# Performance work log

Hardware: AMD Instinct MI355X
Metric: run time of the kernel (lower is better)

The kernel has to match this reference:

```python
import jax, jax.numpy as jnp
import numpy as np
from jax import lax

# dims
B, S, NF, E = 128, 256, 32, 4
D, H = 256, 4
DI = 2 * D            # mLSTM inner (up-projection) dim
DHM, DHS = DI // H, D // H
K = 4                 # causal conv kernel size
FF = 352              # gated FFN dim (~4/3 * D, sLSTM block post-FFN)
NE, NP = 100, 6


def _ln(x, g, b, eps=1e-5):
    mu = x.mean(-1, keepdims=True)
    v = x.var(-1, keepdims=True)
    return (x - mu) / jnp.sqrt(v + eps) * g + b


def _cconv(x, w, b):
    # depthwise causal conv1d: x [B,S,C], w [K,C], b [C]
    k = w.shape[0]
    xp = jnp.pad(x, ((0, 0), (k - 1, 0), (0, 0)))
    y = lax.conv_general_dilated(xp, w[:, None, :], (1,), 'VALID',
                                 dimension_numbers=('NWC', 'WIO', 'NWC'),
                                 feature_group_count=x.shape[-1])
    return y + b


def _headnorm(x, g, b, eps=1e-6):
    # per-head group norm: normalize over last (head-dim) axis
    mu = x.mean(-1, keepdims=True)
    v = x.var(-1, keepdims=True)
    return (x - mu) / jnp.sqrt(v + eps) * g + b


def _forward(emb_esn, emb_prof, W_in, b_in,
             m_ln_g, m_ln_b, m_Wup, m_bup, m_convW, m_convb,
             m_Wq, m_bq, m_Wk, m_bk, m_Wv, m_bv,
             m_Wi, m_bi, m_Wf, m_bf, m_skip, m_ng, m_nb, m_Wdown, m_bdown,
             s_ln_g, s_ln_b, s_convW, s_convb,
             s_Wi, s_bi, s_Wf, s_bf, s_Wz, s_bz, s_Wo, s_bo,
             s_Ri, s_Rf, s_Rz, s_Ro, s_ng, s_nb,
             f_ln_g, f_ln_b, f_Wup, f_bup, f_Wdown, f_bdown,
             h_W1, h_b1, h_W2, h_b2,
             x_sens, x_esn, x_prof):
    Bx, Sx = x_sens.shape[0], x_sens.shape[1]
    ve = jnp.broadcast_to(emb_esn[x_esn][:, None, :], (Bx, Sx, E))
    vp = jnp.broadcast_to(emb_prof[x_prof][:, None, :], (Bx, Sx, E))
    x = jnp.concatenate([x_sens, ve, vp], -1) @ W_in + b_in  # [B,S,D]

    # ---------------- block 0: mLSTM (parallel stabilized matrix memory) ----
    xn = _ln(x, m_ln_g, m_ln_b)
    up = xn @ m_Wup + m_bup
    xm, zg = jnp.split(up, 2, axis=-1)              # [B,S,DI] each
    a = jax.nn.silu(_cconv(xm, m_convW, m_convb))   # causal conv + SiLU
    q = a @ m_Wq + m_bq
    k = a @ m_Wk + m_bk
    v = xm @ m_Wv + m_bv
    gin = jnp.concatenate([q, k, v], -1)            # [B,S,3*DI]
    ipre = (gin @ m_Wi + m_bi).transpose(0, 2, 1)   # [B,H,S]
    fpre = (gin @ m_Wf + m_bf).transpose(0, 2, 1)

    def heads(t, dh):
        return t.reshape(Bx, Sx, H, dh).transpose(0, 2, 1, 3)
    qh, kh, vh = heads(q, DHM), heads(k, DHM), heads(v, DHM)  # [B,H,S,dh]

    lfg = jax.nn.log_sigmoid(fpre)
    F = jnp.cumsum(lfg, -1)                         # [B,H,S]
    logD = F[:, :, :, None] - F[:, :, None, :] + ipre[:, :, None, :]
    mask = jnp.tril(jnp.ones((Sx, Sx), bool))
    logD = jnp.where(mask, logD, -jnp.inf)
    mstab = logD.max(-1, keepdims=True)             # [B,H,S,1]
    Dm = jnp.exp(logD - mstab)
    scores = jnp.einsum('bhtd,bhsd->bhts', qh, kh) / np.sqrt(DHM).astype(np.float32)
    C = scores * Dm
    nrm = jnp.maximum(jnp.abs(C.sum(-1, keepdims=True)), jnp.exp(-mstab))
    hh = jnp.einsum('bhts,bhsd->bhtd', C, vh) / nrm
    hn = _headnorm(hh, m_ng.reshape(1, H, 1, DHM), m_nb.reshape(1, H, 1, DHM))
    hn = hn.transpose(0, 2, 1, 3).reshape(Bx, Sx, DI)
    hn = hn + m_skip * a                            # learnable skip from conv branch
    x = x + (hn * jax.nn.silu(zg)) @ m_Wdown + m_bdown

    # ---------------- block 1: sLSTM (stabilized scalar recurrent scan) -----
    xn = _ln(x, s_ln_g, s_ln_b)
    ac = jax.nn.silu(_cconv(xn, s_convW, s_convb))
    to_t = lambda t: t.reshape(Bx, Sx, H, DHS).transpose(1, 0, 2, 3)  # [S,B,H,dh]
    it = to_t(ac @ s_Wi + s_bi)
    ft = to_t(ac @ s_Wf + s_bf)
    zt = to_t(xn @ s_Wz + s_bz)
    ot = to_t(xn @ s_Wo + s_bo)

    def step(carry, xs):
        h, c, n, m = carry
        i0, f0, z0, o0 = xs
        ip = i0 + jnp.einsum('bhd,hde->bhe', h, s_Ri)
        fp = f0 + jnp.einsum('bhd,hde->bhe', h, s_Rf)
        zp = jnp.tanh(z0 + jnp.einsum('bhd,hde->bhe', h, s_Rz))
        op = jax.nn.sigmoid(o0 + jnp.einsum('bhd,hde->bhe', h, s_Ro))
        mn = jnp.maximum(fp + m, ip)
        ig = jnp.exp(ip - mn)
        fg = jnp.exp(fp + m - mn)
        c = fg * c + ig * zp
        n = fg * n + ig
        h = op * c / n
        return (h, c, n, mn), h

    init = tuple(jnp.zeros((Bx, H, DHS), x.dtype) for _ in range(4))
    _, hs = lax.scan(step, init, (it, ft, zt, ot))  # hs [S,B,H,dh]
    hs = _headnorm(hs, s_ng.reshape(1, 1, H, DHS), s_nb.reshape(1, 1, H, DHS))
    x = x + hs.transpose(1, 0, 2, 3).reshape(Bx, Sx, D)

    # gated FFN (sLSTM block post-feedforward)
    xn = _ln(x, f_ln_g, f_ln_b)
    g_, u_ = jnp.split(xn @ f_Wup + f_bup, 2, axis=-1)
    x = x + (jax.nn.gelu(g_) * u_) @ f_Wdown + f_bdown

    last = x[:, -1, :]
    return jax.nn.relu(last @ h_W1 + h_b1) @ h_W2 + h_b2


def setup_inputs() -> dict:
    key = jax.random.key(0)
    ks = iter(jax.random.split(key, 64))
    nrm = lambda sh, s=0.02: jax.random.normal(next(ks), sh, jnp.float32) * s
    z = lambda sh: jnp.zeros(sh, jnp.float32)
    o = lambda sh: jnp.ones(sh, jnp.float32)
    return dict(
        x_sens=jax.random.normal(next(ks), (B, S, NF), jnp.float32),
        x_esn=jax.random.randint(next(ks), (B,), 0, NE, jnp.int32),
        x_prof=jax.random.randint(next(ks), (B,), 0, NP, jnp.int32),
        emb_esn=nrm((NE + 1, E)), emb_prof=nrm((NP + 1, E)),
        W_in=nrm((NF + 2 * E, D)), b_in=z((D,)),
        m_ln_g=o((D,)), m_ln_b=z((D,)),
        m_Wup=nrm((D, 2 * DI)), m_bup=z((2 * DI,)),
        m_convW=nrm((K, DI)), m_convb=z((DI,)),
        m_Wq=nrm((DI, DI)), m_bq=z((DI,)),
        m_Wk=nrm((DI, DI)), m_bk=z((DI,)),
        m_Wv=nrm((DI, DI)), m_bv=z((DI,)),
        m_Wi=nrm((3 * DI, H)), m_bi=z((H,)),
        m_Wf=nrm((3 * DI, H)), m_bf=o((H,)),
        m_skip=o((DI,)), m_ng=o((DI,)), m_nb=z((DI,)),
        m_Wdown=nrm((DI, D)), m_bdown=z((D,)),
        s_ln_g=o((D,)), s_ln_b=z((D,)),
        s_convW=nrm((K, D)), s_convb=z((D,)),
        s_Wi=nrm((D, D)), s_bi=z((D,)),
        s_Wf=nrm((D, D)), s_bf=o((D,)),
        s_Wz=nrm((D, D)), s_bz=z((D,)),
        s_Wo=nrm((D, D)), s_bo=z((D,)),
        s_Ri=nrm((H, DHS, DHS)), s_Rf=nrm((H, DHS, DHS)),
        s_Rz=nrm((H, DHS, DHS)), s_Ro=nrm((H, DHS, DHS)),
        s_ng=o((D,)), s_nb=z((D,)),
        f_ln_g=o((D,)), f_ln_b=z((D,)),
        f_Wup=nrm((D, 2 * FF)), f_bup=z((2 * FF,)),
        f_Wdown=nrm((FF, D)), f_bdown=z((D,)),
        h_W1=nrm((D, 64), 0.05), h_b1=z((64,)),
        h_W2=nrm((64, 3), 0.05), h_b2=z((3,)),
    )


def reference(emb_esn, emb_prof, W_in, b_in,
              m_ln_g, m_ln_b, m_Wup, m_bup, m_convW, m_convb,
              m_Wq, m_bq, m_Wk, m_bk, m_Wv, m_bv,
              m_Wi, m_bi, m_Wf, m_bf, m_skip, m_ng, m_nb, m_Wdown, m_bdown,
              s_ln_g, s_ln_b, s_convW, s_convb,
              s_Wi, s_bi, s_Wf, s_bf, s_Wz, s_bz, s_Wo, s_bo,
              s_Ri, s_Rf, s_Rz, s_Ro, s_ng, s_nb,
              f_ln_g, f_ln_b, f_Wup, f_bup, f_Wdown, f_bdown,
              h_W1, h_b1, h_W2, h_b2,
              x_sens, x_esn, x_prof):
    return _forward(emb_esn, emb_prof, W_in, b_in,
                    m_ln_g, m_ln_b, m_Wup, m_bup, m_convW, m_convb,
                    m_Wq, m_bq, m_Wk, m_bk, m_Wv, m_bv,
                    m_Wi, m_bi, m_Wf, m_bf, m_skip, m_ng, m_nb, m_Wdown, m_bdown,
                    s_ln_g, s_ln_b, s_convW, s_convb,
                    s_Wi, s_bi, s_Wf, s_bf, s_Wz, s_bz, s_Wo, s_bo,
                    s_Ri, s_Rf, s_Rz, s_Ro, s_ng, s_nb,
                    f_ln_g, f_ln_b, f_Wup, f_bup, f_Wdown, f_bdown,
                    h_W1, h_b1, h_W2, h_b2,
                    x_sens, x_esn, x_prof)
```

## Files before the change

kernel.cpp:

```cpp
#include <hip/hip_runtime.h>
#include <cstdint>
#include <cstddef>


using u16 = unsigned short;
using u32 = unsigned int;

typedef __attribute__((ext_vector_type(8))) short short8;
typedef __attribute__((ext_vector_type(8))) unsigned short ushort8v;
typedef __attribute__((ext_vector_type(4))) float float4v;

#define DEVINL __device__ __forceinline__

DEVINL float b2f(u16 u){ u32 x = ((u32)u) << 16; return __builtin_bit_cast(float, x); }
DEVINL u16 f2b(float f){
  u32 x = __builtin_bit_cast(u32, f);
  u32 r = x + 0x7FFFu + ((x >> 16) & 1u);
  return (u16)(r >> 16);
}
DEVINL float ldval(float x){ return x; }
DEVINL float ldval(u16 x){ return b2f(x); }
DEVINL void stval(float* p, float v){ *p = v; }
DEVINL void stval(u16* p, float v){ *p = f2b(v); }

constexpr int IN_N = 56;
constexpr long long IN_SIZES[IN_N] = {
  1048576, 128, 128, 404, 28, 10240, 256, 256, 256,
  262144, 1024, 2048, 512,
  262144, 512, 262144, 512, 262144, 512,
  6144, 4, 6144, 4,
  512, 512, 512, 131072, 256,
  256, 256, 1024, 256,
  65536, 256, 65536, 256, 65536, 256, 65536, 256,
  16384, 16384, 16384, 16384,
  256, 256,
  256, 256, 180224, 704, 90112, 256,
  16384, 64, 192, 3 };

constexpr bool is_wt_input(int i){
  return i==9 || i==13 || i==15 || i==17 || i==26 || i==32 || i==34 || i==36
      || i==38 || i==48 || i==50;
}

struct CvOff { long long off[IN_N+1]; };
constexpr CvOff make_off(){
  CvOff o{};
  long long a = 0;
  for (int i = 0; i < IN_N; i++){
    o.off[i] = a;
    long long s = IN_SIZES[i];
    if (i == 1 || i == 2 || is_wt_input(i)) s = 0;
    a += s;
  }
  o.off[IN_N] = a;
  return o;
}
constexpr CvOff CVOFF = make_off();
constexpr long long CV_TOTAL = CVOFF.off[IN_N];

constexpr int WT_NW = 11;
constexpr int WTB_IN[WT_NW] = {9, 13, 15, 17, 26, 32, 34, 36, 38, 48, 50};
constexpr int WTB_K[WT_NW]  = {256,512,512,512,512,256,256,256,256,256,352};
constexpr int WTB_N[WT_NW]  = {1024,512,512,512,256,256,256,256,256,704,256};
constexpr long long WTO[WT_NW+1] = {0, 262144, 524288, 786432, 1048576, 1179648,
  1245184, 1310720, 1376256, 1441792, 1622016, 1712128};
constexpr long long WT_ELEMS = WTO[WT_NW];

constexpr long long alignup(long long x){ return ((x + 255) / 256) * 256; }
constexpr long long TOK = 32768;
constexpr long long OFF_FLAG = alignup(CV_TOTAL);
constexpr long long OFF_IP  = OFF_FLAG + 64;
constexpr long long OFF_FP  = OFF_IP  + 131072;
constexpr long long OFF_F   = OFF_FP  + 131072;
constexpr long long OFF_G   = OFF_F   + 131072;
constexpr long long OFF_M   = OFF_G   + 131072;
constexpr long long OFF_X   = OFF_M   + 131072;
constexpr long long OFF_XN  = OFF_X   + TOK*256;
constexpr long long OFF_UP  = OFF_XN  + TOK*128;
constexpr long long OFF_A   = OFF_UP  + TOK*512;
constexpr long long OFF_Q   = OFF_A   + TOK*256;
constexpr long long OFF_K   = OFF_Q   + TOK*256;
constexpr long long OFF_V   = OFF_K   + TOK*256;
constexpr long long OFF_WT  = OFF_V   + TOK*256;
constexpr long long WS_END  = OFF_WT  + WT_ELEMS/2 + 256;


__global__ void detect_kernel(const void* mlng, int* flag){
  if (threadIdx.x == 0){
    u32 u = *(const u32*)mlng;
    *flag = (u == 0x3F803F80u) ? 1 : 0;
  }
}

struct InPtrs { const void* p[IN_N]; };

__global__ __launch_bounds__(256) void convert_kernel(InPtrs ptrs, float* __restrict__ cv,
                                                      const int* __restrict__ flag){
  long long gid = (long long)blockIdx.x * 256 + threadIdx.x;
  if (gid >= CV_TOTAL) return;
  int seg = 0;
#pragma unroll
  for (int i = 1; i < IN_N; i++) seg += (gid >= CVOFF.off[i]) ? 1 : 0;
  long long local = gid - CVOFF.off[seg];
  float v;
  if (*flag) v = b2f(((const u16*)ptrs.p[seg])[local]);
  else       v = ((const float*)ptrs.p[seg])[local];
  cv[gid] = v;
}

__global__ __launch_bounds__(256) void wtrans_kernel(InPtrs ptrs, u16* __restrict__ WTb,
                                                     const int* __restrict__ flag){
  int wz = blockIdx.z;
  int K = WTB_K[wz], N = WTB_N[wz];
  int n0 = blockIdx.x * 32, k0 = blockIdx.y * 32;
  if (n0 >= N || k0 >= K) return;
  const void* W = ptrs.p[WTB_IN[wz]];
  u16* WT = WTb + WTO[wz];
  __shared__ u16 tile[32][34];
  int tx = threadIdx.x & 31, ty = threadIdx.x >> 5;
  bool bf = (*flag != 0);
#pragma unroll
  for (int i = 0; i < 4; i++){
    size_t src = (size_t)(k0 + ty + i*8)*N + n0 + tx;
    tile[ty + i*8][tx] = bf ? ((const u16*)W)[src] : f2b(((const float*)W)[src]);
  }
  __syncthreads();
#pragma unroll
  for (int i = 0; i < 4; i++)
    WT[(size_t)(n0 + ty + i*8)*K + k0 + tx] = tile[tx][ty + i*8];
}

__global__ __launch_bounds__(256) void cat_kernel(const float* __restrict__ xs,
    const int* __restrict__ xe, const int* __restrict__ xp,
    const float* __restrict__ ee, const float* __restrict__ ep,
    float* __restrict__ CAT){
  int gid = blockIdx.x * 256 + threadIdx.x;
  int c = gid % 40; int t = gid / 40; int b = t >> 8;
  float v;
  if (c < 32)      v = xs[(size_t)t*32 + c];
  else if (c < 36) v = ee[xe[b]*4 + (c - 32)];
  else             v = ep[xp[b]*4 + (c - 36)];
  CAT[(size_t)t*40 + c] = v;
}

template<typename TA, typename TC>
__global__ __launch_bounds__(256) void gemm_kernel(
    const TA* __restrict__ A, int lda,
    const float* __restrict__ Wm, const float* __restrict__ bias,
    TC* __restrict__ Cc, int ldc, const float* __restrict__ resid,
    int M, int N, int K)
{
  __shared__ float As[16][68];
  __shared__ float Bs[16][68];
  const int bm = blockIdx.y * 64, bn = blockIdx.x * 64;
  const int tid = threadIdx.x, tx = tid & 15, ty = tid >> 4;
  float acc[4][4] = {};
  for (int k0 = 0; k0 < K; k0 += 16){
#pragma unroll
    for (int i = 0; i < 4; i++){
      int idx = tid + i*256;
      int m = idx >> 4, kq = idx & 15;
      As[kq][m] = (k0 + kq < K) ? ldval(A[(size_t)(bm + m)*lda + k0 + kq]) : 0.f;
      int kk = idx >> 6, n = idx & 63;
      Bs[kk][n] = (k0 + kk < K) ? Wm[(size_t)(k0 + kk)*N + bn + n] : 0.f;
    }
    __syncthreads();
#pragma unroll
    for (int kq = 0; kq < 16; kq++){
      float av[4], bv[4];
#pragma unroll
      for (int i = 0; i < 4; i++) av[i] = As[kq][ty*4 + i];
#pragma unroll
      for (int j = 0; j < 4; j++) bv[j] = Bs[kq][tx*4 + j];
#pragma unroll
      for (int i = 0; i < 4; i++)
#pragma unroll
        for (int j = 0; j < 4; j++) acc[i][j] += av[i]*bv[j];
    }
    __syncthreads();
  }
#pragma unroll
  for (int i = 0; i < 4; i++){
    int m = bm + ty*4 + i;
#pragma unroll
    for (int j = 0; j < 4; j++){
      int n = bn + tx*4 + j;
      float v = acc[i][j] + bias[n];
      if (resid) v += resid[(size_t)m*ldc + n];
      stval(&Cc[(size_t)m*ldc + n], v);
    }
  }
}

template<typename TC>
__global__ __launch_bounds__(256) void gemm_mfma(
    const u16* __restrict__ A, int lda,
    const u16* __restrict__ WT,
    const float* __restrict__ bias,
    TC* __restrict__ Cc, int ldc, const float* __restrict__ resid,
    int N, int K)
{
  __shared__ alignas(16) u16 As[128*40];
  __shared__ alignas(16) u16 Bs[128*40];
  const int bm = blockIdx.y * 128, bn = blockIdx.x * 128;
  const int tid = threadIdx.x;
  const int w = tid >> 6, lane = tid & 63, lm = lane & 15, q = lane >> 4;
  const int wm = w >> 1, wn = w & 1;
  float4v acc[4][4] = {};
  for (int k0 = 0; k0 < K; k0 += 32){
    __syncthreads();
#pragma unroll
    for (int c = tid; c < 512; c += 256){
      int r = c >> 2, ch = c & 3;
      *(uint4*)&As[r*40 + ch*8] = *(const uint4*)&A[(size_t)(bm + r)*lda + k0 + ch*8];
      int n = bn + r;
      uint4 bv = {0u,0u,0u,0u};
      if (n < N) bv = *(const uint4*)&WT[(size_t)n*K + k0 + ch*8];
      *(uint4*)&Bs[r*40 + ch*8] = bv;
    }
    __syncthreads();
    short8 a[4], b[4];
#pragma unroll
    for (int i = 0; i < 4; i++)
      a[i] = *(const short8*)&As[(wm*64 + i*16 + lm)*40 + q*8];
#pragma unroll
    for (int j = 0; j < 4; j++)
      b[j] = *(const short8*)&Bs[(wn*64 + j*16 + lm)*40 + q*8];
#pragma unroll
    for (int i = 0; i < 4; i++)
#pragma unroll
      for (int j = 0; j < 4; j++)
        acc[i][j] = __builtin_amdgcn_mfma_f32_16x16x32_bf16(a[i], b[j], acc[i][j], 0, 0, 0);
  }
#pragma unroll
  for (int i = 0; i < 4; i++){
#pragma unroll
    for (int j = 0; j < 4; j++){
      int col = bn + wn*64 + j*16 + lm;
      if (col < N){
#pragma unroll
        for (int r = 0; r < 4; r++){
          int row = bm + wm*64 + i*16 + q*4 + r;
          float v = acc[i][j][r] + bias[col];
          if (resid) v += resid[(size_t)row*ldc + col];
          stval(&Cc[(size_t)row*ldc + col], v);
        }
      }
    }
  }
}

__global__ __launch_bounds__(256) void ln_kernel(const float* __restrict__ Xin,
    const float* __restrict__ g, const float* __restrict__ b,
    u16* __restrict__ out, float eps){
  int t = blockIdx.x*4 + (threadIdx.x >> 6);
  int e = threadIdx.x & 63;
  float4 v = *(const float4*)&Xin[(size_t)t*256 + e*4];
  float su = v.x + v.y + v.z + v.w;
#pragma unroll
  for (int o = 32; o > 0; o >>= 1) su += __shfl_xor(su, o, 64);
  float mu = su * (1.f/256.f);
  float d0 = v.x - mu, d1 = v.y - mu, d2 = v.z - mu, d3 = v.w - mu;
  float sq = d0*d0 + d1*d1 + d2*d2 + d3*d3;
#pragma unroll
  for (int o = 32; o > 0; o >>= 1) sq += __shfl_xor(sq, o, 64);
  float rstd = rsqrtf(sq * (1.f/256.f) + eps);
  float4 gv = *(const float4*)&g[e*4];
  float4 bv = *(const float4*)&b[e*4];
  ushort4 o4;
  o4.x = f2b(d0*rstd*gv.x + bv.x);
  o4.y = f2b(d1*rstd*gv.y + bv.y);
  o4.z = f2b(d2*rstd*gv.z + bv.z);
  o4.w = f2b(d3*rstd*gv.w + bv.w);
  *(ushort4*)&out[(size_t)t*256 + e*4] = o4;
}

__global__ __launch_bounds__(256) void conv_silu_kernel(const u16* __restrict__ Xc, int ldx, int C,
    const float* __restrict__ w, const float* __restrict__ bias, u16* __restrict__ Y){
  int nc = C >> 3;
  long long gid = (long long)blockIdx.x * 256 + threadIdx.x;
  int c8 = (int)(gid % nc) * 8; long long t = gid / nc;
  int s = (int)(t & 255);
  float acc[8];
#pragma unroll
  for (int i = 0; i < 8; i++) acc[i] = bias[c8 + i];
#pragma unroll
  for (int j = 0; j < 4; j++){
    int so = s - 3 + j;
    if (so >= 0){
      ushort8v xv = *(const ushort8v*)&Xc[(size_t)(t - 3 + j)*ldx + c8];
#pragma unroll
      for (int i = 0; i < 8; i++) acc[i] += b2f(xv[i]) * w[j*C + c8 + i];
    }
  }
  ushort8v o8;
#pragma unroll
  for (int i = 0; i < 8; i++) o8[i] = f2b(acc[i] / (1.f + __expf(-acc[i])));
  *(ushort8v*)&Y[(size_t)t*C + c8] = o8;
}

__global__ __launch_bounds__(256) void gates_kernel(
    const u16* __restrict__ Q, const u16* __restrict__ Kb, const u16* __restrict__ V,
    const float* __restrict__ Wi, const float* __restrict__ bi,
    const float* __restrict__ Wf, const float* __restrict__ bf,
    float* __restrict__ IP, float* __restrict__ FP){
  int t = blockIdx.x; int tid = threadIdx.x;
  int o = tid & 7, seg = tid >> 3;
  int b = t >> 8, s = t & 255;
  int g = o & 3;
  const float* Wg = (o >= 4) ? Wf : Wi;
  float part = 0.f;
#pragma unroll
  for (int i = 0; i < 6; i++){
    int k8 = seg*48 + i*8;
    const u16* src; int off;
    if (k8 < 512){ src = Q; off = k8; }
    else if (k8 < 1024){ src = Kb; off = k8 - 512; }
    else { src = V; off = k8 - 1024; }
    ushort8v gv = *(const ushort8v*)&src[(size_t)t*512 + off];
#pragma unroll
    for (int j = 0; j < 8; j++) part += b2f(gv[j]) * Wg[(k8 + j)*4 + g];
  }
  __shared__ float red[256];
  red[tid] = part; __syncthreads();
  if (tid < 8){
    float tot = 0.f;
    for (int ss = 0; ss < 32; ss++) tot += red[ss*8 + tid];
    int gg = tid & 3;
    if (tid < 4) IP[(b*4 + gg)*256 + s] = tot + bi[gg];
    else         FP[(b*4 + gg)*256 + s] = tot + bf[gg];
  }
}

__global__ __launch_bounds__(256) void fscan_kernel(const float* __restrict__ IP,
    const float* __restrict__ FP, float* __restrict__ Fo, float* __restrict__ Go,
    float* __restrict__ Mo){
  int bh = blockIdx.x; int s = threadIdx.x;
  int idx = bh*256 + s;
  __shared__ float buf[256];
  float fp = FP[idx];
  float lfg = fminf(fp, 0.f) - log1pf(expf(-fabsf(fp)));
  float v = lfg;
  buf[s] = v; __syncthreads();
  for (int off = 1; off < 256; off <<= 1){
    float tv = (s >= off) ? buf[s - off] : 0.f;
    __syncthreads();
    v += tv; buf[s] = v;
    __syncthreads();
  }
  float Fv = v;
  float g = IP[idx] - Fv;
  float mv = g;
  buf[s] = mv; __syncthreads();
  for (int off = 1; off < 256; off <<= 1){
    float tv = (s >= off) ? buf[s - off] : -3.0e38f;
    __syncthreads();
    mv = fmaxf(mv, tv); buf[s] = mv;
    __syncthreads();
  }
  Fo[idx] = Fv; Go[idx] = g; Mo[idx] = mv;
}

__global__ __launch_bounds__(256) void attn_kernel(
    const u16* __restrict__ Q, const u16* __restrict__ Kb, const u16* __restrict__ V,
    const float* __restrict__ G, const float* __restrict__ Mx, const float* __restrict__ F,
    const u16* __restrict__ Ab, const u16* __restrict__ UPb,
    const float* __restrict__ ng, const float* __restrict__ nb,
    const float* __restrict__ skip, u16* __restrict__ Yb)
{
  int bh = blockIdx.y, b = bh >> 2, h = bh & 3;
  int tt = blockIdx.x, t0 = tt * 64;
  int tid = threadIdx.x;
  int w = tid >> 6, lane = tid & 63, lm = lane & 15, q = lane >> 4;
  int gbase = bh * 256;

  __shared__ alignas(16) u16 Qs[64*136];
  __shared__ alignas(16) u16 Ks[64*136];
  __shared__ alignas(16) u16 Vt[128*72];
  __shared__ alignas(16) u16 Ps[64*72];
  __shared__ float rs[64];

#pragma unroll
  for (int c = tid; c < 1024; c += 256){
    int r = c >> 4, ch = c & 15;
    *(uint4*)&Qs[r*136 + ch*8] =
      *(const uint4*)&Q[((size_t)(b*256 + t0 + r))*512 + h*128 + ch*8];
  }
  if (tid < 64) rs[tid] = 0.f;

  float mrow[4];
#pragma unroll
  for (int r = 0; r < 4; r++) mrow[r] = Mx[gbase + t0 + w*16 + q*4 + r];

  float4v acc2[8] = {};
  const float scale = 0.08838834764831845f;

  for (int ss = 0; ss <= tt; ss++){
    int s0 = ss * 64;
    __syncthreads();
#pragma unroll
    for (int c = tid; c < 1024; c += 256){
      int r = c >> 4, ch = c & 15;
      *(uint4*)&Ks[r*136 + ch*8] =
        *(const uint4*)&Kb[((size_t)(b*256 + s0 + r))*512 + h*128 + ch*8];
    }
#pragma unroll
    for (int c = tid; c < 1024; c += 256){
      int sl = c & 63, db = c >> 6;
      ushort8v v = *(const ushort8v*)&V[((size_t)(b*256 + s0 + sl))*512 + h*128 + db*8];
#pragma unroll
      for (int j = 0; j < 8; j++) Vt[(db*8 + j)*72 + sl] = v[j];
    }
    __syncthreads();
    float4v sacc[4] = {};
#pragma unroll
    for (int k0 = 0; k0 < 128; k0 += 32){
      short8 a = *(const short8*)&Qs[(w*16 + lm)*136 + k0 + q*8];
#pragma unroll
      for (int j = 0; j < 4; j++){
        short8 bb = *(const short8*)&Ks[(j*16 + lm)*136 + k0 + q*8];
        sacc[j] = __builtin_amdgcn_mfma_f32_16x16x32_bf16(a, bb, sacc[j], 0, 0, 0);
      }
    }
    float rp[4] = {0.f, 0.f, 0.f, 0.f};
#pragma unroll
    for (int j = 0; j < 4; j++){
      int scol = s0 + j*16 + lm;
      float gq = G[gbase + scol];
#pragma unroll
      for (int r = 0; r < 4; r++){
        int trow = t0 + w*16 + q*4 + r;
        float cval = (scol <= trow) ? sacc[j][r]*scale*__expf(gq - mrow[r]) : 0.f;
        Ps[(w*16 + q*4 + r)*72 + j*16 + lm] = f2b(cval);
        rp[r] += cval;
      }
    }
#pragma unroll
    for (int r = 0; r < 4; r++){
#pragma unroll
      for (int m = 1; m < 16; m <<= 1) rp[r] += __shfl_xor(rp[r], m, 16);
      if (lm == 0) rs[w*16 + q*4 + r] += rp[r];
    }
#pragma unroll
    for (int k0 = 0; k0 < 64; k0 += 32){
      short8 a = *(const short8*)&Ps[(w*16 + lm)*72 + k0 + q*8];
#pragma unroll
      for (int jd = 0; jd < 8; jd++){
        short8 bb = *(const short8*)&Vt[(jd*16 + lm)*72 + k0 + q*8];
        acc2[jd] = __builtin_amdgcn_mfma_f32_16x16x32_bf16(a, bb, acc2[jd], 0, 0, 0);
      }
    }
  }
  __syncthreads();
#pragma unroll
  for (int r = 0; r < 4; r++){
    int rl = w*16 + q*4 + r;
    int t = t0 + rl;
    float Fv = F[gbase + t];
    float nrm = fmaxf(fabsf(rs[rl]), __expf(-(Fv + mrow[r])));
    float inv = 1.f / nrm;
    float vv[8];
    float su = 0.f;
#pragma unroll
    for (int jd = 0; jd < 8; jd++){ vv[jd] = acc2[jd][r]*inv; su += vv[jd]; }
#pragma unroll
    for (int m = 1; m < 16; m <<= 1) su += __shfl_xor(su, m, 16);
    float mu = su * (1.f/128.f);
    float sq = 0.f;
#pragma unroll
    for (int jd = 0; jd < 8; jd++){ vv[jd] -= mu; sq += vv[jd]*vv[jd]; }
#pragma unroll
    for (int m = 1; m < 16; m <<= 1) sq += __shfl_xor(sq, m, 16);
    float rstd = rsqrtf(sq * (1.f/128.f) + 1e-6f);
#pragma unroll
    for (int jd = 0; jd < 8; jd++){
      int c = h*128 + jd*16 + lm;
      float hv = vv[jd]*rstd*ng[c] + nb[c];
      float av = b2f(Ab[(size_t)t*512 + c]);
      float zg = b2f(UPb[(size_t)t*1024 + 512 + c]);
      float sz = zg / (1.f + __expf(-zg));
      Yb[(size_t)t*512 + c] = f2b((hv + skip[c]*av)*sz);
    }
  }
}

__global__ __launch_bounds__(320) void scan_kernel(
    const float* __restrict__ IT, const float* __restrict__ FT,
    const float* __restrict__ ZT, const float* __restrict__ OT,
    const float* __restrict__ Ri, const float* __restrict__ Rf,
    const float* __restrict__ Rz, const float* __restrict__ Ro,
    const float* __restrict__ sng, const float* __restrict__ snb,
    float* __restrict__ Xr){
  int bh = blockIdx.x; int b = bh >> 2, h = bh & 3;
  int e = threadIdx.x & 63;
  int w = threadIdx.x >> 6;
  __shared__ float4 part[2][4][64];
  __shared__ float hbuf[2][64];
  size_t rowbase = ((size_t)b*256)*256 + h*64 + e;

  if (w < 4){
    float r0[16], r1[16], r2[16], r3[16];
    const float* Rp0 = Ri + h*4096 + w*1024;
    const float* Rp1 = Rf + h*4096 + w*1024;
    const float* Rp2 = Rz + h*4096 + w*1024;
    const float* Rp3 = Ro + h*4096 + w*1024;
#pragma unroll
    for (int d = 0; d < 16; d++){
      r0[d] = Rp0[d*64 + e];
      r1[d] = Rp1[d*64 + e];
      r2[d] = Rp2[d*64 + e];
      r3[d] = Rp3[d*64 + e];
    }
    float hS = 0.f, cS = 0.f, nS = 0.f, mS = 0.f;
    float i0 = 0.f, f0 = 0.f, z0 = 0.f, o0 = 0.f;
    if (w == 0){ i0 = IT[rowbase]; f0 = FT[rowbase]; z0 = ZT[rowbase]; o0 = OT[rowbase]; }
    for (int s = 0; s < 256; s++){
      float iN = 0.f, fN = 0.f, zN = 0.f, oN = 0.f;
      if (w == 0 && s < 255){
        size_t nr = rowbase + (size_t)(s + 1)*256;
        iN = IT[nr]; fN = FT[nr]; zN = ZT[nr]; oN = OT[nr];
      }
      float ai0 = 0.f, ai1 = 0.f, af0 = 0.f, af1 = 0.f;
      float az0 = 0.f, az1 = 0.f, ao0 = 0.f, ao1 = 0.f;
#pragma unroll
      for (int k = 0; k < 16; k += 2){
        float h0 = __builtin_bit_cast(float,
            __builtin_amdgcn_readlane(__builtin_bit_cast(int, hS), w*16 + k));
        float h1 = __builtin_bit_cast(float,
            __builtin_amdgcn_readlane(__builtin_bit_cast(int, hS), w*16 + k + 1));
        ai0 += h0*r0[k]; ai1 += h1*r0[k+1];
        af0 += h0*r1[k]; af1 += h1*r1[k+1];
        az0 += h0*r2[k]; az1 += h1*r2[k+1];
        ao0 += h0*r3[k]; ao1 += h1*r3[k+1];
      }
      float4 p;
      p.x = ai0 + ai1; p.y = af0 + af1; p.z = az0 + az1; p.w = ao0 + ao1;
      if (w == 0){
        p.x += i0; p.y += f0; p.z += z0; p.w += o0;
        i0 = iN; f0 = fN; z0 = zN; o0 = oN;
      }
      part[s & 1][w][e] = p;
      __syncthreads();
      float4 q0 = part[s & 1][0][e];
      float4 q1 = part[s & 1][1][e];
      float4 q2 = part[s & 1][2][e];
      float4 q3 = part[s & 1][3][e];
      float ip = q0.x + q1.x + q2.x + q3.x;
      float fp = q0.y + q1.y + q2.y + q3.y;
      float zr = q0.z + q1.z + q2.z + q3.z;
      float og = q0.w + q1.w + q2.w + q3.w;
      float zp = 1.f - 2.f*__builtin_amdgcn_rcpf(__expf(2.f*zr) + 1.f);
      float op = __builtin_amdgcn_rcpf(1.f + __expf(-og));
      float mn = fmaxf(fp + mS, ip);
      float ig = __expf(ip - mn);
      float fg = __expf(fp + mS - mn);
      cS = fg*cS + ig*zp;
      nS = fg*nS + ig;
      mS = mn;
      hS = op * cS * __builtin_amdgcn_rcpf(nS);
      if (w == 1) hbuf[s & 1][e] = hS;
    }
    __syncthreads();
  } else {
    float gw = sng[h*64 + e], bw = snb[h*64 + e];
    float xp = 0.f, xc = 0.f;
    for (int s = 0; s < 256; s++){
      xc = Xr[rowbase + (size_t)s*256];
      __syncthreads();
      if (s > 0){
        float hv = hbuf[(s - 1) & 1][e];
        float su = hv, sq = hv*hv;
#pragma unroll
        for (int o = 32; o > 0; o >>= 1){
          su += __shfl_xor(su, o, 64);
          sq += __shfl_xor(sq, o, 64);
        }
        float mu = su * (1.f/64.f);
        float var = fmaxf(sq * (1.f/64.f) - mu*mu, 0.f);
        float nv = (hv - mu) * rsqrtf(var + 1e-6f) * gw + bw;
        Xr[rowbase + (size_t)(s - 1)*256] = xp + nv;
      }
      xp = xc;
    }
    __syncthreads();
    float hv = hbuf[1][e];
    float su = hv, sq = hv*hv;
#pragma unroll
    for (int o = 32; o > 0; o >>= 1){
      su += __shfl_xor(su, o, 64);
      sq += __shfl_xor(sq, o, 64);
    }
    float mu = su * (1.f/64.f);
    float var = fmaxf(sq * (1.f/64.f) - mu*mu, 0.f);
    float nv = (hv - mu) * rsqrtf(var + 1e-6f) * gw + bw;
    Xr[rowbase + (size_t)255*256] = xp + nv;
  }
}

__global__ __launch_bounds__(256) void ffn_act_kernel(const u16* __restrict__ GU,
                                                      u16* __restrict__ P){
  long long gid = (long long)blockIdx.x * 256 + threadIdx.x;
  int j8 = (int)(gid % 44) * 8; long long t = gid / 44;
  ushort8v gv = *(const ushort8v*)&GU[(size_t)t*704 + j8];
  ushort8v uv = *(const ushort8v*)&GU[(size_t)t*704 + 352 + j8];
  ushort8v o8;
#pragma unroll
  for (int i = 0; i < 8; i++){
    float g = b2f(gv[i]);
    float u = b2f(uv[i]);
    float inner = 0.7978845608028654f * (g + 0.044715f*g*g*g);
    float gel = 0.5f * g * (1.f + tanhf(inner));
    o8[i] = f2b(gel * u);
  }
  *(ushort8v*)&P[(size_t)t*352 + j8] = o8;
}

__global__ __launch_bounds__(64) void head_kernel(const float* __restrict__ X,
    const float* __restrict__ W1, const float* __restrict__ b1,
    const float* __restrict__ W2, const float* __restrict__ b2,
    void* out, const int* __restrict__ flag){
  int b = blockIdx.x, j = threadIdx.x;
  __shared__ float L[256];
  __shared__ float H1[64];
  for (int i = j; i < 256; i += 64) L[i] = X[((size_t)(b*256 + 255))*256 + i];
  __syncthreads();
  float acc = b1[j];
  for (int d = 0; d < 256; d++) acc += L[d] * W1[d*64 + j];
  H1[j] = fmaxf(acc, 0.f);
  __syncthreads();
  if (j < 3){
    float o = b2[j];
    for (int k2 = 0; k2 < 64; k2++) o += H1[k2] * W2[k2*3 + j];
    if (*flag) ((u16*)out)[b*3 + j] = f2b(o);
    else       ((float*)out)[b*3 + j] = o;
  }
}

extern "C" void kernel_launch(void* const* d_in, const int* in_sizes, int n_in,
                              void* d_out, int out_size, void* d_ws, size_t ws_size,
                              hipStream_t stream)
{
  if (n_in != IN_N) return;
  for (int i = 0; i < IN_N; i++) if ((long long)in_sizes[i] != IN_SIZES[i]) return;
  if (ws_size < (size_t)WS_END * 4) return;
  if (out_size != 384) return;

  float* ws = (float*)d_ws;
  float* cv = ws;
  auto cvp = [&](int i){ return cv + CVOFF.off[i]; };

  int*   flag = (int*)(ws + OFF_FLAG);
  float* IP   = ws + OFF_IP;
  float* FP   = ws + OFF_FP;
  float* Fb   = ws + OFF_F;
  float* Gb   = ws + OFF_G;
  float* Mb   = ws + OFF_M;
  float* X    = ws + OFF_X;
  u16*   XNb  = (u16*)(ws + OFF_XN);
  u16*   UPb  = (u16*)(ws + OFF_UP);
  u16*   Ab   = (u16*)(ws + OFF_A);
  u16*   Qb   = (u16*)(ws + OFF_Q);
  u16*   Kbb  = (u16*)(ws + OFF_K);
  u16*   Vb   = (u16*)(ws + OFF_V);
  u16*   WTb  = (u16*)(ws + OFF_WT);
  float* CAT = ws + OFF_V;
  u16*   Yb  = Qb;
  u16*   ACb = Ab;
  float* ITf = ws + OFF_K;
  float* FTf = ws + OFF_V;
  float* ZTf = ws + OFF_Q;
  float* OTf = ws + OFF_UP;
  u16*   GUb = UPb;
  u16*   Pb  = Ab;

  auto wt = [&](int widx){ return WTb + WTO[widx]; };

  InPtrs ptrs;
  for (int i = 0; i < IN_N; i++) ptrs.p[i] = d_in[i];

  const int M = 32768;
  detect_kernel<<<1, 64, 0, stream>>>(d_in[7], flag);
  int cvblocks = (int)((CV_TOTAL + 255) / 256);
  convert_kernel<<<cvblocks, 256, 0, stream>>>(ptrs, cv, flag);
  wtrans_kernel<<<dim3(32, 16, 11), 256, 0, stream>>>(ptrs, WTb, flag);
  cat_kernel<<<5120, 256, 0, stream>>>(cvp(0), (const int*)d_in[1], (const int*)d_in[2],
                                       cvp(3), cvp(4), CAT);
  gemm_kernel<float, float><<<dim3(4, 512), 256, 0, stream>>>(CAT, 40, cvp(5), cvp(6),
      X, 256, nullptr, M, 256, 40);
  ln_kernel<<<8192, 256, 0, stream>>>(X, cvp(7), cvp(8), XNb, 1e-5f);
  gemm_mfma<u16><<<dim3(8, 256), 256, 0, stream>>>(XNb, 256, wt(0), cvp(10),
      UPb, 1024, nullptr, 1024, 256);
  conv_silu_kernel<<<8192, 256, 0, stream>>>(UPb, 1024, 512, cvp(11), cvp(12), Ab);
  gemm_mfma<u16><<<dim3(4, 256), 256, 0, stream>>>(Ab, 512, wt(1), cvp(14),
      Qb, 512, nullptr, 512, 512);
  gemm_mfma<u16><<<dim3(4, 256), 256, 0, stream>>>(Ab, 512, wt(2), cvp(16),
      Kbb, 512, nullptr, 512, 512);
  gemm_mfma<u16><<<dim3(4, 256), 256, 0, stream>>>(UPb, 1024, wt(3), cvp(18),
      Vb, 512, nullptr, 512, 512);
  gates_kernel<<<M, 256, 0, stream>>>(Qb, Kbb, Vb, cvp(19), cvp(20), cvp(21), cvp(22), IP, FP);
  fscan_kernel<<<512, 256, 0, stream>>>(IP, FP, Fb, Gb, Mb);
  attn_kernel<<<dim3(4, 512), 256, 0, stream>>>(Qb, Kbb, Vb, Gb, Mb, Fb,
      Ab, UPb, cvp(24), cvp(25), cvp(23), Yb);
  gemm_mfma<float><<<dim3(2, 256), 256, 0, stream>>>(Yb, 512, wt(4), cvp(27),
      X, 256, X, 256, 512);
  ln_kernel<<<8192, 256, 0, stream>>>(X, cvp(28), cvp(29), XNb, 1e-5f);
  conv_silu_kernel<<<4096, 256, 0, stream>>>(XNb, 256, 256, cvp(30), cvp(31), ACb);
  gemm_mfma<float><<<dim3(2, 256), 256, 0, stream>>>(ACb, 256, wt(5), cvp(33),
      ITf, 256, nullptr, 256, 256);
  gemm_mfma<float><<<dim3(2, 256), 256, 0, stream>>>(ACb, 256, wt(6), cvp(35),
      FTf, 256, nullptr, 256, 256);
  gemm_mfma<float><<<dim3(2, 256), 256, 0, stream>>>(XNb, 256, wt(7), cvp(37),
      ZTf, 256, nullptr, 256, 256);
  gemm_mfma<float><<<dim3(2, 256), 256, 0, stream>>>(XNb, 256, wt(8), cvp(39),
      OTf, 256, nullptr, 256, 256);
  scan_kernel<<<512, 320, 0, stream>>>(ITf, FTf, ZTf, OTf, cvp(40), cvp(41), cvp(42), cvp(43),
      cvp(44), cvp(45), X);
  ln_kernel<<<8192, 256, 0, stream>>>(X, cvp(46), cvp(47), XNb, 1e-5f);
  gemm_mfma<u16><<<dim3(6, 256), 256, 0, stream>>>(XNb, 256, wt(9), cvp(49),
      GUb, 704, nullptr, 704, 256);
  ffn_act_kernel<<<5632, 256, 0, stream>>>(GUb, Pb);
  gemm_mfma<float><<<dim3(2, 256), 256, 0, stream>>>(Pb, 352, wt(10), cvp(51),
      X, 256, X, 256, 352);
  head_kernel<<<128, 64, 0, stream>>>(X, cvp(52), cvp(53), cvp(54), cvp(55), d_out, flag);
}
```

Baseline: 1.137 ms.

## Chunk sLSTM scan gate loads and headnorm writeback in 16-step blocks

```diff
diff --git a/kernel.cpp b/kernel.cpp
--- a/kernel.cpp
+++ b/kernel.cpp
@@ -22,6 +22,30 @@
 DEVINL float ldval(u16 x){ return b2f(x); }
 DEVINL void stval(float* p, float v){ *p = v; }
 DEVINL void stval(u16* p, float v){ *p = f2b(v); }
+
+DEVINL void dpp_sum2(float a, float b, float& oa, float& ob){
+  int xa, xb;
+  xa = __builtin_amdgcn_update_dpp(0, __builtin_bit_cast(int, a), 0x111, 0xf, 0xf, true);
+  xb = __builtin_amdgcn_update_dpp(0, __builtin_bit_cast(int, b), 0x111, 0xf, 0xf, true);
+  a += __builtin_bit_cast(float, xa); b += __builtin_bit_cast(float, xb);
+  xa = __builtin_amdgcn_update_dpp(0, __builtin_bit_cast(int, a), 0x112, 0xf, 0xf, true);
+  xb = __builtin_amdgcn_update_dpp(0, __builtin_bit_cast(int, b), 0x112, 0xf, 0xf, true);
+  a += __builtin_bit_cast(float, xa); b += __builtin_bit_cast(float, xb);
+  xa = __builtin_amdgcn_update_dpp(0, __builtin_bit_cast(int, a), 0x114, 0xf, 0xf, true);
+  xb = __builtin_amdgcn_update_dpp(0, __builtin_bit_cast(int, b), 0x114, 0xf, 0xf, true);
+  a += __builtin_bit_cast(float, xa); b += __builtin_bit_cast(float, xb);
+  xa = __builtin_amdgcn_update_dpp(0, __builtin_bit_cast(int, a), 0x118, 0xf, 0xf, true);
+  xb = __builtin_amdgcn_update_dpp(0, __builtin_bit_cast(int, b), 0x118, 0xf, 0xf, true);
+  a += __builtin_bit_cast(float, xa); b += __builtin_bit_cast(float, xb);
+  xa = __builtin_amdgcn_update_dpp(0, __builtin_bit_cast(int, a), 0x142, 0xf, 0xf, true);
+  xb = __builtin_amdgcn_update_dpp(0, __builtin_bit_cast(int, b), 0x142, 0xf, 0xf, true);
+  a += __builtin_bit_cast(float, xa); b += __builtin_bit_cast(float, xb);
+  xa = __builtin_amdgcn_update_dpp(0, __builtin_bit_cast(int, a), 0x143, 0xf, 0xf, true);
+  xb = __builtin_amdgcn_update_dpp(0, __builtin_bit_cast(int, b), 0x143, 0xf, 0xf, true);
+  a += __builtin_bit_cast(float, xa); b += __builtin_bit_cast(float, xb);
+  oa = __builtin_bit_cast(float, __builtin_amdgcn_readlane(__builtin_bit_cast(int, a), 63));
+  ob = __builtin_bit_cast(float, __builtin_amdgcn_readlane(__builtin_bit_cast(int, b), 63));
+}
 
 constexpr int IN_N = 56;
 constexpr long long IN_SIZES[IN_N] = {
@@ -495,7 +519,7 @@
   int e = threadIdx.x & 63;
   int w = threadIdx.x >> 6;
   __shared__ float4 part[2][4][64];
-  __shared__ float hbuf[2][64];
+  __shared__ float hbuf[32][64];
   size_t rowbase = ((size_t)b*256)*256 + h*64 + e;
 
   if (w < 4){
@@ -511,89 +535,100 @@
       r2[d] = Rp2[d*64 + e];
       r3[d] = Rp3[d*64 + e];
     }
+    const float* Gp = (w == 0) ? IT : (w == 1) ? FT : (w == 2) ? ZT : OT;
     float hS = 0.f, cS = 0.f, nS = 0.f, mS = 0.f;
-    float i0 = 0.f, f0 = 0.f, z0 = 0.f, o0 = 0.f;
-    if (w == 0){ i0 = IT[rowbase]; f0 = FT[rowbase]; z0 = ZT[rowbase]; o0 = OT[rowbase]; }
-    for (int s = 0; s < 256; s++){
-      float iN = 0.f, fN = 0.f, zN = 0.f, oN = 0.f;
-      if (w == 0 && s < 255){
-        size_t nr = rowbase + (size_t)(s + 1)*256;
-        iN = IT[nr]; fN = FT[nr]; zN = ZT[nr]; oN = OT[nr];
+    for (int c = 0; c < 16; c++){
+      float gch[16];
+#pragma unroll
+      for (int j = 0; j < 16; j++)
+        gch[j] = Gp[rowbase + (size_t)(c*16 + j)*256];
+#pragma unroll
+      for (int j = 0; j < 16; j++){
+        float ai0 = 0.f, ai1 = 0.f, af0 = 0.f, af1 = 0.f;
+        float az0 = 0.f, az1 = 0.f, ao0 = 0.f, ao1 = 0.f;
+#pragma unroll
+        for (int k = 0; k < 16; k += 2){
+          float h0 = __builtin_bit_cast(float,
+              __builtin_amdgcn_readlane(__builtin_bit_cast(int, hS), w*16 + k));
+          float h1 = __builtin_bit_cast(float,
+              __builtin_amdgcn_readlane(__builtin_bit_cast(int, hS), w*16 + k + 1));
+          ai0 += h0*r0[k]; ai1 += h1*r0[k+1];
+          af0 += h0*r1[k]; af1 += h1*r1[k+1];
+          az0 += h0*r2[k]; az1 += h1*r2[k+1];
+          ao0 += h0*r3[k]; ao1 += h1*r3[k+1];
+        }
+        float4 p;
+        p.x = ai0 + ai1; p.y = af0 + af1; p.z = az0 + az1; p.w = ao0 + ao1;
+        float g = gch[j];
+        if      (w == 0) p.x += g;
+        else if (w == 1) p.y += g;
+        else if (w == 2) p.z += g;
+        else             p.w += g;
+        part[j & 1][w][e] = p;
+        __syncthreads();
+        float4 q0 = part[j & 1][0][e];
+        float4 q1 = part[j & 1][1][e];
+        float4 q2 = part[j & 1][2][e];
+        float4 q3 = part[j & 1][3][e];
+        float ip = (q0.x + q1.x) + (q2.x + q3.x);
+        float fp = (q0.y + q1.y) + (q2.y + q3.y);
+        float zr = (q0.z + q1.z) + (q2.z + q3.z);
+        float og = (q0.w + q1.w) + (q2.w + q3.w);
+        float zp = 1.f - 2.f*__builtin_amdgcn_rcpf(__expf(2.f*zr) + 1.f);
+        float op = __builtin_amdgcn_rcpf(1.f + __expf(-og));
+        float mn = fmaxf(fp + mS, ip);
+        float ig = __expf(ip - mn);
+        float fg = __expf(fp + mS - mn);
+        cS = fg*cS + ig*zp;
+        nS = fg*nS + ig;
+        mS = mn;
+        hS = op * cS * __builtin_amdgcn_rcpf(nS);
+        if (w == 1) hbuf[((c & 1) << 4) | j][e] = hS;
       }
-      float ai0 = 0.f, ai1 = 0.f, af0 = 0.f, af1 = 0.f;
-      float az0 = 0.f, az1 = 0.f, ao0 = 0.f, ao1 = 0.f;
-#pragma unroll
-      for (int k = 0; k < 16; k += 2){
-        float h0 = __builtin_bit_cast(float,
-            __builtin_amdgcn_readlane(__builtin_bit_cast(int, hS), w*16 + k));
-        float h1 = __builtin_bit_cast(float,
-            __builtin_amdgcn_readlane(__builtin_bit_cast(int, hS), w*16 + k + 1));
-        ai0 += h0*r0[k]; ai1 += h1*r0[k+1];
-        af0 += h0*r1[k]; af1 += h1*r1[k+1];
-        az0 += h0*r2[k]; az1 += h1*r2[k+1];
-        ao0 += h0*r3[k]; ao1 += h1*r3[k+1];
-      }
-      float4 p;
-      p.x = ai0 + ai1; p.y = af0 + af1; p.z = az0 + az1; p.w = ao0 + ao1;
-      if (w == 0){
-        p.x += i0; p.y += f0; p.z += z0; p.w += o0;
-        i0 = iN; f0 = fN; z0 = zN; o0 = oN;
-      }
-      part[s & 1][w][e] = p;
-      __syncthreads();
-      float4 q0 = part[s & 1][0][e];
-      float4 q1 = part[s & 1][1][e];
-      float4 q2 = part[s & 1][2][e];
-      float4 q3 = part[s & 1][3][e];
-      float ip = q0.x + q1.x + q2.x + q3.x;
-      float fp = q0.y + q1.y + q2.y + q3.y;
-      float zr = q0.z + q1.z + q2.z + q3.z;
-      float og = q0.w + q1.w + q2.w + q3.w;
-      float zp = 1.f - 2.f*__builtin_amdgcn_rcpf(__expf(2.f*zr) + 1.f);
-      float op = __builtin_amdgcn_rcpf(1.f + __expf(-og));
-      float mn = fmaxf(fp + mS, ip);
-      float ig = __expf(ip - mn);
-      float fg = __expf(fp + mS - mn);
-      cS = fg*cS + ig*zp;
-      nS = fg*nS + ig;
-      mS = mn;
-      hS = op * cS * __builtin_amdgcn_rcpf(nS);
-      if (w == 1) hbuf[s & 1][e] = hS;
     }
     __syncthreads();
   } else {
     float gw = sng[h*64 + e], bw = snb[h*64 + e];
-    float xp = 0.f, xc = 0.f;
-    for (int s = 0; s < 256; s++){
-      xc = Xr[rowbase + (size_t)s*256];
-      __syncthreads();
-      if (s > 0){
-        float hv = hbuf[(s - 1) & 1][e];
-        float su = hv, sq = hv*hv;
-#pragma unroll
-        for (int o = 32; o > 0; o >>= 1){
-          su += __shfl_xor(su, o, 64);
-          sq += __shfl_xor(sq, o, 64);
+    for (int c = 0; c < 16; c++){
+      float xch[16], och[16];
+      if (c > 0){
+#pragma unroll
+        for (int j = 0; j < 16; j++)
+          xch[j] = Xr[rowbase + (size_t)((c - 1)*16 + j)*256];
+      }
+#pragma unroll
+      for (int j = 0; j < 16; j++){
+        if (c > 0){
+          float hv = hbuf[(((c - 1) & 1) << 4) | j][e];
+          float su, sq;
+          dpp_sum2(hv, hv*hv, su, sq);
+          float mu = su * (1.f/64.f);
+          float var = fmaxf(sq * (1.f/64.f) - mu*mu, 0.f);
+          och[j] = xch[j] + (hv - mu) * rsqrtf(var + 1e-6f) * gw + bw;
+          if (j == 15){
+#pragma unroll
+            for (int jj = 0; jj < 16; jj++)
+              Xr[rowbase + (size_t)((c - 1)*16 + jj)*256] = och[jj];
+          }
         }
-        float mu = su * (1.f/64.f);
-        float var = fmaxf(sq * (1.f/64.f) - mu*mu, 0.f);
-        float nv = (hv - mu) * rsqrtf(var + 1e-6f) * gw + bw;
-        Xr[rowbase + (size_t)(s - 1)*256] = xp + nv;
+        __syncthreads();
       }
-      xp = xc;
-    }
-    __syncthreads();
-    float hv = hbuf[1][e];
-    float su = hv, sq = hv*hv;
-#pragma unroll
-    for (int o = 32; o > 0; o >>= 1){
-      su += __shfl_xor(su, o, 64);
-      sq += __shfl_xor(sq, o, 64);
-    }
-    float mu = su * (1.f/64.f);
-    float var = fmaxf(sq * (1.f/64.f) - mu*mu, 0.f);
-    float nv = (hv - mu) * rsqrtf(var + 1e-6f) * gw + bw;
-    Xr[rowbase + (size_t)255*256] = xp + nv;
+    }
+    __syncthreads();
+    float xch[16];
+#pragma unroll
+    for (int j = 0; j < 16; j++)
+      xch[j] = Xr[rowbase + (size_t)(240 + j)*256];
+#pragma unroll
+    for (int j = 0; j < 16; j++){
+      float hv = hbuf[16 | j][e];
+      float su, sq;
+      dpp_sum2(hv, hv*hv, su, sq);
+      float mu = su * (1.f/64.f);
+      float var = fmaxf(sq * (1.f/64.f) - mu*mu, 0.f);
+      Xr[rowbase + (size_t)(240 + j)*256] =
+          xch[j] + (hv - mu) * rsqrtf(var + 1e-6f) * gw + bw;
+    }
   }
 }
 
```

Result: slower. 1.163 ms (+2.3%).

## Merge sLSTM gate GEMMs pairwise and spread gate loads across scan waves

Applied to the files above, without the earlier changes.

```diff
diff --git a/kernel.cpp b/kernel.cpp
--- a/kernel.cpp
+++ b/kernel.cpp
@@ -22,6 +22,37 @@
 DEVINL float ldval(u16 x){ return b2f(x); }
 DEVINL void stval(float* p, float v){ *p = v; }
 DEVINL void stval(u16* p, float v){ *p = f2b(v); }
+
+DEVINL void lds_barrier(){
+  asm volatile("s_waitcnt lgkmcnt(0)" ::: "memory");
+  __builtin_amdgcn_sched_barrier(0);
+  __builtin_amdgcn_s_barrier();
+  __builtin_amdgcn_sched_barrier(0);
+}
+
+DEVINL void dpp_sum2(float a, float b, float& oa, float& ob){
+  int xa, xb;
+  xa = __builtin_amdgcn_update_dpp(0, __builtin_bit_cast(int, a), 0x111, 0xf, 0xf, true);
+  xb = __builtin_amdgcn_update_dpp(0, __builtin_bit_cast(int, b), 0x111, 0xf, 0xf, true);
+  a += __builtin_bit_cast(float, xa); b += __builtin_bit_cast(float, xb);
+  xa = __builtin_amdgcn_update_dpp(0, __builtin_bit_cast(int, a), 0x112, 0xf, 0xf, true);
+  xb = __builtin_amdgcn_update_dpp(0, __builtin_bit_cast(int, b), 0x112, 0xf, 0xf, true);
+  a += __builtin_bit_cast(float, xa); b += __builtin_bit_cast(float, xb);
+  xa = __builtin_amdgcn_update_dpp(0, __builtin_bit_cast(int, a), 0x114, 0xf, 0xf, true);
+  xb = __builtin_amdgcn_update_dpp(0, __builtin_bit_cast(int, b), 0x114, 0xf, 0xf, true);
+  a += __builtin_bit_cast(float, xa); b += __builtin_bit_cast(float, xb);
+  xa = __builtin_amdgcn_update_dpp(0, __builtin_bit_cast(int, a), 0x118, 0xf, 0xf, true);
+  xb = __builtin_amdgcn_update_dpp(0, __builtin_bit_cast(int, b), 0x118, 0xf, 0xf, true);
+  a += __builtin_bit_cast(float, xa); b += __builtin_bit_cast(float, xb);
+  xa = __builtin_amdgcn_update_dpp(0, __builtin_bit_cast(int, a), 0x142, 0xf, 0xf, true);
+  xb = __builtin_amdgcn_update_dpp(0, __builtin_bit_cast(int, b), 0x142, 0xf, 0xf, true);
+  a += __builtin_bit_cast(float, xa); b += __builtin_bit_cast(float, xb);
+  xa = __builtin_amdgcn_update_dpp(0, __builtin_bit_cast(int, a), 0x143, 0xf, 0xf, true);
+  xb = __builtin_amdgcn_update_dpp(0, __builtin_bit_cast(int, b), 0x143, 0xf, 0xf, true);
+  a += __builtin_bit_cast(float, xa); b += __builtin_bit_cast(float, xb);
+  oa = __builtin_bit_cast(float, __builtin_amdgcn_readlane(__builtin_bit_cast(int, a), 63));
+  ob = __builtin_bit_cast(float, __builtin_amdgcn_readlane(__builtin_bit_cast(int, b), 63));
+}
 
 constexpr int IN_N = 56;
 constexpr long long IN_SIZES[IN_N] = {
@@ -485,8 +516,7 @@
 }
 
 __global__ __launch_bounds__(320) void scan_kernel(
-    const float* __restrict__ IT, const float* __restrict__ FT,
-    const float* __restrict__ ZT, const float* __restrict__ OT,
+    const float* __restrict__ G1, const float* __restrict__ G2,
     const float* __restrict__ Ri, const float* __restrict__ Rf,
     const float* __restrict__ Rz, const float* __restrict__ Ro,
     const float* __restrict__ sng, const float* __restrict__ snb,
@@ -496,7 +526,7 @@
   int w = threadIdx.x >> 6;
   __shared__ float4 part[2][4][64];
   __shared__ float hbuf[2][64];
-  size_t rowbase = ((size_t)b*256)*256 + h*64 + e;
+  size_t xrow = ((size_t)b*256)*256 + h*64 + e;
 
   if (w < 4){
     float r0[16], r1[16], r2[16], r3[16];
@@ -511,15 +541,14 @@
       r2[d] = Rp2[d*64 + e];
       r3[d] = Rp3[d*64 + e];
     }
+    const float* Gp = (w < 2) ? G1 : G2;
+    size_t grow = ((size_t)b*256)*512 + ((w & 1) ? 256 : 0) + h*64 + e;
     float hS = 0.f, cS = 0.f, nS = 0.f, mS = 0.f;
-    float i0 = 0.f, f0 = 0.f, z0 = 0.f, o0 = 0.f;
-    if (w == 0){ i0 = IT[rowbase]; f0 = FT[rowbase]; z0 = ZT[rowbase]; o0 = OT[rowbase]; }
+    float gv = Gp[grow];
+    float gn = Gp[grow + 512];
     for (int s = 0; s < 256; s++){
-      float iN = 0.f, fN = 0.f, zN = 0.f, oN = 0.f;
-      if (w == 0 && s < 255){
-        size_t nr = rowbase + (size_t)(s + 1)*256;
-        iN = IT[nr]; fN = FT[nr]; zN = ZT[nr]; oN = OT[nr];
-      }
+      float gn2 = 0.f;
+      if (s < 254) gn2 = Gp[grow + (size_t)(s + 2)*512];
       float ai0 = 0.f, ai1 = 0.f, af0 = 0.f, af1 = 0.f;
       float az0 = 0.f, az1 = 0.f, ao0 = 0.f, ao1 = 0.f;
 #pragma unroll
@@ -535,20 +564,20 @@
       }
       float4 p;
       p.x = ai0 + ai1; p.y = af0 + af1; p.z = az0 + az1; p.w = ao0 + ao1;
-      if (w == 0){
-        p.x += i0; p.y += f0; p.z += z0; p.w += o0;
-        i0 = iN; f0 = fN; z0 = zN; o0 = oN;
-      }
+      if      (w == 0) p.x += gv;
+      else if (w == 1) p.y += gv;
+      else if (w == 2) p.z += gv;
+      else             p.w += gv;
       part[s & 1][w][e] = p;
-      __syncthreads();
+      lds_barrier();
       float4 q0 = part[s & 1][0][e];
       float4 q1 = part[s & 1][1][e];
       float4 q2 = part[s & 1][2][e];
       float4 q3 = part[s & 1][3][e];
-      float ip = q0.x + q1.x + q2.x + q3.x;
-      float fp = q0.y + q1.y + q2.y + q3.y;
-      float zr = q0.z + q1.z + q2.z + q3.z;
-      float og = q0.w + q1.w + q2.w + q3.w;
+      float ip = (q0.x + q1.x) + (q2.x + q3.x);
+      float fp = (q0.y + q1.y) + (q2.y + q3.y);
+      float zr = (q0.z + q1.z) + (q2.z + q3.z);
+      float og = (q0.w + q1.w) + (q2.w + q3.w);
       float zp = 1.f - 2.f*__builtin_amdgcn_rcpf(__expf(2.f*zr) + 1.f);
       float op = __builtin_amdgcn_rcpf(1.f + __expf(-og));
       float mn = fmaxf(fp + mS, ip);
@@ -559,41 +588,34 @@
       mS = mn;
       hS = op * cS * __builtin_amdgcn_rcpf(nS);
       if (w == 1) hbuf[s & 1][e] = hS;
-    }
-    __syncthreads();
+      gv = gn; gn = gn2;
+    }
+    lds_barrier();
   } else {
     float gw = sng[h*64 + e], bw = snb[h*64 + e];
     float xp = 0.f, xc = 0.f;
     for (int s = 0; s < 256; s++){
-      xc = Xr[rowbase + (size_t)s*256];
-      __syncthreads();
+      xc = Xr[xrow + (size_t)s*256];
+      lds_barrier();
       if (s > 0){
         float hv = hbuf[(s - 1) & 1][e];
-        float su = hv, sq = hv*hv;
-#pragma unroll
-        for (int o = 32; o > 0; o >>= 1){
-          su += __shfl_xor(su, o, 64);
-          sq += __shfl_xor(sq, o, 64);
-        }
+        float su, sq;
+        dpp_sum2(hv, hv*hv, su, sq);
         float mu = su * (1.f/64.f);
         float var = fmaxf(sq * (1.f/64.f) - mu*mu, 0.f);
         float nv = (hv - mu) * rsqrtf(var + 1e-6f) * gw + bw;
-        Xr[rowbase + (size_t)(s - 1)*256] = xp + nv;
+        Xr[xrow + (size_t)(s - 1)*256] = xp + nv;
       }
       xp = xc;
     }
-    __syncthreads();
+    lds_barrier();
     float hv = hbuf[1][e];
-    float su = hv, sq = hv*hv;
-#pragma unroll
-    for (int o = 32; o > 0; o >>= 1){
-      su += __shfl_xor(su, o, 64);
-      sq += __shfl_xor(sq, o, 64);
-    }
+    float su, sq;
+    dpp_sum2(hv, hv*hv, su, sq);
     float mu = su * (1.f/64.f);
     float var = fmaxf(sq * (1.f/64.f) - mu*mu, 0.f);
     float nv = (hv - mu) * rsqrtf(var + 1e-6f) * gw + bw;
-    Xr[rowbase + (size_t)255*256] = xp + nv;
+    Xr[xrow + (size_t)255*256] = xp + nv;
   }
 }
 
@@ -666,10 +688,8 @@
   float* CAT = ws + OFF_V;
   u16*   Yb  = Qb;
   u16*   ACb = Ab;
-  float* ITf = ws + OFF_K;
-  float* FTf = ws + OFF_V;
-  float* ZTf = ws + OFF_Q;
-  float* OTf = ws + OFF_UP;
+  float* G1f = ws + OFF_K;
+  float* G2f = ws + OFF_UP;
   u16*   GUb = UPb;
   u16*   Pb  = Ab;
 
@@ -705,15 +725,11 @@
       X, 256, X, 256, 512);
   ln_kernel<<<8192, 256, 0, stream>>>(X, cvp(28), cvp(29), XNb, 1e-5f);
   conv_silu_kernel<<<4096, 256, 0, stream>>>(XNb, 256, 256, cvp(30), cvp(31), ACb);
-  gemm_mfma<float><<<dim3(2, 256), 256, 0, stream>>>(ACb, 256, wt(5), cvp(33),
-      ITf, 256, nullptr, 256, 256);
-  gemm_mfma<float><<<dim3(2, 256), 256, 0, stream>>>(ACb, 256, wt(6), cvp(35),
-      FTf, 256, nullptr, 256, 256);
-  gemm_mfma<float><<<dim3(2, 256), 256, 0, stream>>>(XNb, 256, wt(7), cvp(37),
-      ZTf, 256, nullptr, 256, 256);
-  gemm_mfma<float><<<dim3(2, 256), 256, 0, stream>>>(XNb, 256, wt(8), cvp(39),
-      OTf, 256, nullptr, 256, 256);
-  scan_kernel<<<512, 320, 0, stream>>>(ITf, FTf, ZTf, OTf, cvp(40), cvp(41), cvp(42), cvp(43),
+  gemm_mfma<float><<<dim3(4, 256), 256, 0, stream>>>(ACb, 256, wt(5), cvp(33),
+      G1f, 512, nullptr, 512, 256);
+  gemm_mfma<float><<<dim3(4, 256), 256, 0, stream>>>(XNb, 256, wt(7), cvp(37),
+      G2f, 512, nullptr, 512, 256);
+  scan_kernel<<<512, 320, 0, stream>>>(G1f, G2f, cvp(40), cvp(41), cvp(42), cvp(43),
       cvp(44), cvp(45), X);
   ln_kernel<<<8192, 256, 0, stream>>>(X, cvp(46), cvp(47), XNb, 1e-5f);
   gemm_mfma<u16><<<dim3(6, 256), 256, 0, stream>>>(XNb, 256, wt(9), cvp(49),
```

After: 1.152 ms. Within noise of the previous version (+1.4%).
